# Kernel tuning notes

Hardware: AMD Instinct MI355X
Metric: run time of the kernel (lower is better)

Reference implementation:

```python
import jax, jax.numpy as jnp
import numpy as np

G = 8          # group (window) size -> N = G*G = 64
HEADS = 8
DIM = 256
HEAD_DIM = DIM // HEADS
SCALE = HEAD_DIM ** -0.5
POS_DIM = (DIM // 4) // 4  # 16
LN_EPS = 1e-5


def _make_bias_tables():
    # biases: coordinates (1-g..g-1) x (1-g..g-1) -> [(2g-1)^2, 2] float
    r = np.arange(1 - G, G)
    bh, bw = np.meshgrid(r, r, indexing='ij')
    biases = np.stack([bh.ravel(), bw.ravel()], axis=1).astype(np.float32)
    # relative position index [g^2, g^2]
    ch, cw = np.meshgrid(np.arange(G), np.arange(G), indexing='ij')
    coords = np.stack([ch.ravel(), cw.ravel()])              # [2, g^2]
    rel = coords[:, :, None] - coords[:, None, :]            # [2, g^2, g^2]
    rel = rel.transpose(1, 2, 0)
    rel[:, :, 0] += G - 1
    rel[:, :, 1] += G - 1
    rel[:, :, 0] *= 2 * G - 1
    rel_idx = rel.sum(-1).astype(np.int32)                   # [g^2, g^2]
    return biases, rel_idx


def setup_inputs() -> dict:
    key = jax.random.key(0)
    ks = jax.random.split(key, 8)
    B, N, C = 2048, G * G, DIM
    biases_np, rel_idx_np = _make_bias_tables()
    s = lambda fan: 1.0 / np.sqrt(fan)
    return {
        'x': jax.random.normal(ks[0], (B, N, C), jnp.float32),
        'qkv_w': jax.random.normal(ks[1], (C, 3 * C), jnp.float32) * s(C),
        'qkv_b': jnp.zeros((3 * C,), jnp.float32),
        'proj_w': jax.random.normal(ks[2], (C, C), jnp.float32) * s(C),
        'proj_b': jnp.zeros((C,), jnp.float32),
        'pos_proj_w': jax.random.normal(ks[3], (2, POS_DIM), jnp.float32) * s(2),
        'pos_proj_b': jnp.zeros((POS_DIM,), jnp.float32),
        'ln1_g': jnp.ones((POS_DIM,), jnp.float32), 'ln1_b': jnp.zeros((POS_DIM,), jnp.float32),
        'fc1_w': jax.random.normal(ks[4], (POS_DIM, POS_DIM), jnp.float32) * s(POS_DIM),
        'fc1_b': jnp.zeros((POS_DIM,), jnp.float32),
        'ln2_g': jnp.ones((POS_DIM,), jnp.float32), 'ln2_b': jnp.zeros((POS_DIM,), jnp.float32),
        'fc2_w': jax.random.normal(ks[5], (POS_DIM, POS_DIM), jnp.float32) * s(POS_DIM),
        'fc2_b': jnp.zeros((POS_DIM,), jnp.float32),
        'ln3_g': jnp.ones((POS_DIM,), jnp.float32), 'ln3_b': jnp.zeros((POS_DIM,), jnp.float32),
        'fc3_w': jax.random.normal(ks[6], (POS_DIM, HEADS), jnp.float32) * s(POS_DIM),
        'fc3_b': jnp.zeros((HEADS,), jnp.float32),
        'biases': jnp.asarray(biases_np),
        'rel_idx': jnp.asarray(rel_idx_np),
    }


def _ln(h, g, b):
    m = jnp.mean(h, -1, keepdims=True)
    v = jnp.mean((h - m) ** 2, -1, keepdims=True)
    return (h - m) * jax.lax.rsqrt(v + LN_EPS) * g + b


def reference(x, qkv_w, qkv_b, proj_w, proj_b,
              pos_proj_w, pos_proj_b,
              ln1_g, ln1_b, fc1_w, fc1_b,
              ln2_g, ln2_b, fc2_w, fc2_b,
              ln3_g, ln3_b, fc3_w, fc3_b,
              biases, rel_idx):
    B, N, C = x.shape
    # dynamic position bias MLP: [(2g-1)^2, 2] -> [(2g-1)^2, heads]
    h = biases @ pos_proj_w + pos_proj_b
    h = jax.nn.relu(_ln(h, ln1_g, ln1_b)) @ fc1_w + fc1_b
    h = jax.nn.relu(_ln(h, ln2_g, ln2_b)) @ fc2_w + fc2_b
    pos = jax.nn.relu(_ln(h, ln3_g, ln3_b)) @ fc3_w + fc3_b        # [225, H]
    rel_bias = pos[rel_idx]                                        # [N, N, H]
    rel_bias = jnp.transpose(rel_bias, (2, 0, 1))                  # [H, N, N]

    qkv = (x @ qkv_w + qkv_b).reshape(B, N, 3, HEADS, HEAD_DIM)
    qkv = jnp.transpose(qkv, (2, 0, 3, 1, 4))                      # [3, B, H, N, Dh]
    q, k, v = qkv[0] * SCALE, qkv[1], qkv[2]
    attn = jnp.einsum('bhnd,bhmd->bhnm', q, k) + rel_bias[None]    # [B, H, N, N]
    attn = jax.nn.softmax(attn, axis=-1)
    out = jnp.einsum('bhnm,bhmd->bhnd', attn, v)                   # [B, H, N, Dh]
    out = jnp.transpose(out, (0, 2, 1, 3)).reshape(B, N, C)
    return out @ proj_w + proj_b
```

## Files before the change

### kernel.cpp

```cpp
#include <hip/hip_runtime.h>

typedef _Float16 half_t;
typedef __attribute__((ext_vector_type(8))) _Float16 half8;
typedef __attribute__((ext_vector_type(4))) _Float16 half4;
typedef __attribute__((ext_vector_type(4))) float float4v;

#define LN_EPS 1e-5f
#define QK_SCALE 0.17677669529663687f

static __device__ __forceinline__ float4v mfma16(half8 a, half8 b, float4v c) {
    return __builtin_amdgcn_mfma_f32_16x16x32_f16(a, b, c, 0, 0, 0);
}

static __device__ __forceinline__ int swzA(int row, int colByte) {
    return row * 512 + ((((colByte >> 4) ^ ((row >> 1) & 7)) << 4) | (colByte & 15));
}
static __device__ __forceinline__ int swzB(int row, int colByte) {
    return row * 64 + ((((colByte >> 4) ^ ((row >> 1) & 3)) << 4) | (colByte & 15));
}
static __device__ __forceinline__ int swzC(int row, int colByte) {
    return row * 128 + ((((colByte >> 4) ^ (row & 7)) << 4) | (colByte & 15));
}

static __device__ void ln_relu16(float* h, const float* __restrict__ g, const float* __restrict__ b) {
    float m = 0.f;
    for (int j = 0; j < 16; ++j) m += h[j];
    m *= (1.0f / 16.0f);
    float v = 0.f;
    for (int j = 0; j < 16; ++j) { float d = h[j] - m; v += d * d; }
    v *= (1.0f / 16.0f);
    float rs = rsqrtf(v + LN_EPS);
    for (int j = 0; j < 16; ++j) {
        float t = (h[j] - m) * rs * g[j] + b[j];
        h[j] = t > 0.f ? t : 0.f;
    }
}

__global__ void prep_kernel(
    const float* __restrict__ qkv_w,
    const float* __restrict__ proj_w,
    const float* __restrict__ biases,
    const float* __restrict__ pos_w, const float* __restrict__ pos_b,
    const float* __restrict__ ln1_g, const float* __restrict__ ln1_b,
    const float* __restrict__ fc1_w, const float* __restrict__ fc1_b,
    const float* __restrict__ ln2_g, const float* __restrict__ ln2_b,
    const float* __restrict__ fc2_w, const float* __restrict__ fc2_b,
    const float* __restrict__ ln3_g, const float* __restrict__ ln3_b,
    const float* __restrict__ fc3_w, const float* __restrict__ fc3_b,
    const int* __restrict__ rel_idx,
    half_t* __restrict__ wqkvT,
    half_t* __restrict__ wprojT,
    float* __restrict__ rbp)
{
    __shared__ float tile[64][65];
    __shared__ float pos_s[225][8];
    const int t = blockIdx.x;
    const int tid = threadIdx.x;

    if (t < 64) {
        const float* src; half_t* dst; int ncols, rg, cg;
        if (t < 48) { src = qkv_w;  dst = wqkvT;  ncols = 768; rg = t / 12;      cg = t % 12; }
        else        { src = proj_w; dst = wprojT; ncols = 256; rg = (t-48) >> 2; cg = (t-48) & 3; }
        const int r0 = tid >> 6, c = tid & 63;
        for (int i = 0; i < 16; ++i) {
            int r = i * 4 + r0;
            tile[r][c] = src[(rg * 64 + r) * ncols + cg * 64 + c];
        }
        __syncthreads();
        for (int i = 0; i < 16; ++i) {
            int r = i * 4 + r0;
            dst[(cg * 64 + r) * 256 + rg * 64 + c] = (half_t)tile[c][r];
        }
    } else {
        if (tid < 225) {
            float h[16], h2[16];
            float b0 = biases[tid * 2], b1 = biases[tid * 2 + 1];
            for (int j = 0; j < 16; ++j) h[j] = b0 * pos_w[j] + b1 * pos_w[16 + j] + pos_b[j];
            ln_relu16(h, ln1_g, ln1_b);
            for (int j = 0; j < 16; ++j) {
                float s = fc1_b[j];
                for (int k = 0; k < 16; ++k) s += h[k] * fc1_w[k * 16 + j];
                h2[j] = s;
            }
            ln_relu16(h2, ln2_g, ln2_b);
            for (int j = 0; j < 16; ++j) {
                float s = fc2_b[j];
                for (int k = 0; k < 16; ++k) s += h2[k] * fc2_w[k * 16 + j];
                h[j] = s;
            }
            ln_relu16(h, ln3_g, ln3_b);
            for (int j = 0; j < 8; ++j) {
                float s = fc3_b[j];
                for (int k = 0; k < 16; ++k) s += h[k] * fc3_w[k * 8 + j];
                pos_s[tid][j] = s;
            }
        }
        __syncthreads();
        for (int e = tid; e < 8 * 64 * 64; e += 256) {
            int hh = e >> 12, rem = e & 4095;
            int row = rem >> 6, c = rem & 63;
            int tj = c >> 4, mm = c & 15;
            rbp[hh * 4096 + row * 64 + mm * 4 + tj] = pos_s[rel_idx[row * 64 + c]][hh];
        }
    }
}

__global__ __launch_bounds__(512, 2) void fused_kernel(
    const float* __restrict__ x,
    const half_t* __restrict__ wqkvT,
    const float* __restrict__ qkv_b,
    const half_t* __restrict__ wprojT,
    const float* __restrict__ proj_b,
    const float* __restrict__ rbp,
    float* __restrict__ out)
{
    __shared__ __align__(16) char smem[65536];
    char* xs  = smem;
    char* atn = smem;
    char* arenas = smem + 32768;

    const int b   = blockIdx.x;
    const int tid = threadIdx.x;
    const int w    = tid >> 6;
    const int lane = tid & 63;
    const int m = lane & 15;
    const int g = lane >> 4;
    char* wA  = arenas + w * 4096;
    char* vts = xs + w * 4096;

    const float* xg = x + (size_t)b * 16384;
    #pragma unroll
    for (int i = 0; i < 8; ++i) {
        int u = tid + i * 512;
        int row = u >> 6, c4 = u & 63;
        float4v xv = *(const float4v*)(xg + u * 4);
        half4 hv;
        hv[0] = (half_t)xv[0]; hv[1] = (half_t)xv[1];
        hv[2] = (half_t)xv[2]; hv[3] = (half_t)xv[3];
        *(half4*)(xs + swzA(row, c4 * 8)) = hv;
    }
    __syncthreads();

    float4v qb[2][2];
    #pragma unroll
    for (int pt = 0; pt < 2; ++pt)
        #pragma unroll
        for (int c2 = 0; c2 < 2; ++c2)
            qb[pt][c2] = *(const float4v*)(qkv_b + pt * 256 + w * 32 + c2 * 16 + g * 4);

    half8 aq[4], bk[4];
    {
        float4v qa[2][4], ka[2][4];
        #pragma unroll
        for (int c2 = 0; c2 < 2; ++c2)
            #pragma unroll
            for (int ti = 0; ti < 4; ++ti) {
                qa[c2][ti] = {0.f, 0.f, 0.f, 0.f};
                ka[c2][ti] = {0.f, 0.f, 0.f, 0.f};
            }
        const half_t* wqb = wqkvT + (size_t)(w * 32 + m) * 256 + g * 8;
        #pragma unroll
        for (int kk = 0; kk < 8; ++kk) {
            half8 af[4];
            #pragma unroll
            for (int ti = 0; ti < 4; ++ti)
                af[ti] = *(const half8*)(xs + swzA(ti * 16 + m, kk * 64 + g * 16));
            half8 wq0 = *(const half8*)(wqb + kk * 32);
            half8 wq1 = *(const half8*)(wqb + 16 * 256 + kk * 32);
            half8 wk0 = *(const half8*)(wqb + 256 * 256 + kk * 32);
            half8 wk1 = *(const half8*)(wqb + 272 * 256 + kk * 32);
            #pragma unroll
            for (int ti = 0; ti < 4; ++ti) {
                qa[0][ti] = mfma16(wq0, af[ti], qa[0][ti]);
                qa[1][ti] = mfma16(wq1, af[ti], qa[1][ti]);
                ka[0][ti] = mfma16(wk0, af[ti], ka[0][ti]);
                ka[1][ti] = mfma16(wk1, af[ti], ka[1][ti]);
            }
        }
        #pragma unroll
        for (int c2 = 0; c2 < 2; ++c2)
            #pragma unroll
            for (int ti = 0; ti < 4; ++ti) {
                half4 t;
                #pragma unroll
                for (int r = 0; r < 4; ++r) t[r] = (half_t)(qa[c2][ti][r] + qb[0][c2][r]);
                *(half4*)(wA + ti * 1024 + swzB(m, (c2 * 16 + g * 4) * 2)) = t;
            }
        #pragma unroll
        for (int ti = 0; ti < 4; ++ti)
            aq[ti] = *(const half8*)(wA + ti * 1024 + swzB(m, g * 16));
        __builtin_amdgcn_sched_barrier(0);
        #pragma unroll
        for (int c2 = 0; c2 < 2; ++c2)
            #pragma unroll
            for (int ti = 0; ti < 4; ++ti) {
                half4 t;
                #pragma unroll
                for (int r = 0; r < 4; ++r) t[r] = (half_t)(ka[c2][ti][r] + qb[1][c2][r]);
                *(half4*)(wA + ti * 1024 + swzB(m, (c2 * 16 + g * 4) * 2)) = t;
            }
        #pragma unroll
        for (int ti = 0; ti < 4; ++ti)
            bk[ti] = *(const half8*)(wA + ti * 1024 + swzB(m, g * 16));
        __builtin_amdgcn_sched_barrier(0);
    }

    half4 ph[4][4];
    const float* rbh = rbp + w * 4096;
    #pragma unroll
    for (int ti = 0; ti < 4; ++ti) {
        float4v z = {0.f, 0.f, 0.f, 0.f};
        float4v s0 = mfma16(aq[ti], bk[0], z);
        float4v s1 = mfma16(aq[ti], bk[1], z);
        float4v s2 = mfma16(aq[ti], bk[2], z);
        float4v s3 = mfma16(aq[ti], bk[3], z);
        #pragma unroll
        for (int r = 0; r < 4; ++r) {
            float4v rb = *(const float4v*)(rbh + (ti * 16 + g * 4 + r) * 64 + m * 4);
            float e0 = __expf(s0[r] * QK_SCALE + rb[0]);
            float e1 = __expf(s1[r] * QK_SCALE + rb[1]);
            float e2 = __expf(s2[r] * QK_SCALE + rb[2]);
            float e3 = __expf(s3[r] * QK_SCALE + rb[3]);
            float s = e0 + e1 + e2 + e3;
            s += __shfl_xor(s, 1); s += __shfl_xor(s, 2);
            s += __shfl_xor(s, 4); s += __shfl_xor(s, 8);
            float is = 1.0f / s;
            ph[ti][0][r] = (half_t)(e0 * is);
            ph[ti][1][r] = (half_t)(e1 * is);
            ph[ti][2][r] = (half_t)(e2 * is);
            ph[ti][3][r] = (half_t)(e3 * is);
        }
    }

    half4 vh[2][4];
    {
        float4v va[2][4];
        #pragma unroll
        for (int c2 = 0; c2 < 2; ++c2)
            #pragma unroll
            for (int ti = 0; ti < 4; ++ti) va[c2][ti] = {0.f, 0.f, 0.f, 0.f};
        const half_t* wvb = wqkvT + (size_t)(512 + w * 32 + m) * 256 + g * 8;
        #pragma unroll
        for (int kk = 0; kk < 8; ++kk) {
            half8 wv0 = *(const half8*)(wvb + kk * 32);
            half8 wv1 = *(const half8*)(wvb + 16 * 256 + kk * 32);
            #pragma unroll
            for (int ti = 0; ti < 4; ++ti) {
                half8 af = *(const half8*)(xs + swzA(ti * 16 + m, kk * 64 + g * 16));
                va[0][ti] = mfma16(af, wv0, va[0][ti]);
                va[1][ti] = mfma16(af, wv1, va[1][ti]);
            }
        }
        float vb0 = qkv_b[512 + w * 32 + m], vb1 = qkv_b[512 + w * 32 + 16 + m];
        #pragma unroll
        for (int c2 = 0; c2 < 2; ++c2)
            #pragma unroll
            for (int ti = 0; ti < 4; ++ti)
                #pragma unroll
                for (int r = 0; r < 4; ++r)
                    vh[c2][ti][r] = (half_t)(va[c2][ti][r] + (c2 ? vb1 : vb0));
    }
    __syncthreads();

    #pragma unroll
    for (int c2 = 0; c2 < 2; ++c2)
        #pragma unroll
        for (int ti = 0; ti < 4; ++ti)
            *(half4*)(vts + swzC(c2 * 16 + m, ti * 32 + g * 8)) = vh[c2][ti];

    float4v oacc[2][4];
    #pragma unroll
    for (int tjd = 0; tjd < 2; ++tjd)
        #pragma unroll
        for (int ti = 0; ti < 4; ++ti) oacc[tjd][ti] = {0.f, 0.f, 0.f, 0.f};
    #pragma unroll
    for (int nc = 0; nc < 2; ++nc) {
        #pragma unroll
        for (int ti = 0; ti < 4; ++ti)
            #pragma unroll
            for (int t2 = 0; t2 < 2; ++t2)
                #pragma unroll
                for (int r = 0; r < 4; ++r)
                    *(half_t*)(wA + swzB(ti * 16 + g * 4 + r, (t2 * 16 + m) * 2)) =
                        ph[ti][nc * 2 + t2][r];
        half8 pa[4];
        #pragma unroll
        for (int ti = 0; ti < 4; ++ti)
            pa[ti] = *(const half8*)(wA + swzB(ti * 16 + m, g * 16));
        #pragma unroll
        for (int tjd = 0; tjd < 2; ++tjd) {
            half8 bv = *(const half8*)(vts + swzC(tjd * 16 + m, nc * 64 + g * 16));
            #pragma unroll
            for (int ti = 0; ti < 4; ++ti)
                oacc[tjd][ti] = mfma16(pa[ti], bv, oacc[tjd][ti]);
        }
        __builtin_amdgcn_sched_barrier(0);
    }
    __syncthreads();

    #pragma unroll
    for (int tjd = 0; tjd < 2; ++tjd)
        #pragma unroll
        for (int ti = 0; ti < 4; ++ti)
            #pragma unroll
            for (int r = 0; r < 4; ++r)
                *(half_t*)(atn + swzA(ti * 16 + g * 4 + r, (w * 32 + tjd * 16 + m) * 2)) =
                    (half_t)oacc[tjd][ti][r];
    __syncthreads();

    float* og = out + (size_t)b * 16384;
    const int oc0 = w * 32;
    float4v pacc[2][4];
    #pragma unroll
    for (int c2 = 0; c2 < 2; ++c2)
        #pragma unroll
        for (int ti = 0; ti < 4; ++ti) pacc[c2][ti] = {0.f, 0.f, 0.f, 0.f};
    const half_t* wpb = wprojT + (size_t)(oc0 + m) * 256 + g * 8;
    #pragma unroll
    for (int kk = 0; kk < 8; ++kk) {
        half8 wf0 = *(const half8*)(wpb + kk * 32);
        half8 wf1 = *(const half8*)(wpb + 16 * 256 + kk * 32);
        #pragma unroll
        for (int ti = 0; ti < 4; ++ti) {
            half8 af = *(const half8*)(atn + swzA(ti * 16 + m, kk * 64 + g * 16));
            pacc[0][ti] = mfma16(af, wf0, pacc[0][ti]);
            pacc[1][ti] = mfma16(af, wf1, pacc[1][ti]);
        }
    }
    float pb0 = proj_b[oc0 + m], pb1 = proj_b[oc0 + 16 + m];
    #pragma unroll
    for (int c2 = 0; c2 < 2; ++c2)
        #pragma unroll
        for (int ti = 0; ti < 4; ++ti)
            #pragma unroll
            for (int r = 0; r < 4; ++r)
                og[(ti * 16 + g * 4 + r) * 256 + oc0 + c2 * 16 + m] =
                    pacc[c2][ti][r] + (c2 ? pb1 : pb0);
}

extern "C" void kernel_launch(void* const* d_in, const int* in_sizes, int n_in,
                              void* d_out, int out_size, void* d_ws, size_t ws_size,
                              hipStream_t stream) {
    const float* x          = (const float*)d_in[0];
    const float* qkv_w      = (const float*)d_in[1];
    const float* qkv_b      = (const float*)d_in[2];
    const float* proj_w     = (const float*)d_in[3];
    const float* proj_b     = (const float*)d_in[4];
    const float* pos_proj_w = (const float*)d_in[5];
    const float* pos_proj_b = (const float*)d_in[6];
    const float* ln1_g = (const float*)d_in[7];
    const float* ln1_b = (const float*)d_in[8];
    const float* fc1_w = (const float*)d_in[9];
    const float* fc1_b = (const float*)d_in[10];
    const float* ln2_g = (const float*)d_in[11];
    const float* ln2_b = (const float*)d_in[12];
    const float* fc2_w = (const float*)d_in[13];
    const float* fc2_b = (const float*)d_in[14];
    const float* ln3_g = (const float*)d_in[15];
    const float* ln3_b = (const float*)d_in[16];
    const float* fc3_w = (const float*)d_in[17];
    const float* fc3_b = (const float*)d_in[18];
    const float* biases = (const float*)d_in[19];
    const int*  rel_idx = (const int*)d_in[20];

    half_t* wqkvT  = (half_t*)d_ws;
    half_t* wprojT = (half_t*)((char*)d_ws + 393216);
    float*  rbp    = (float*)((char*)d_ws + 524288);

    const int B = in_sizes[0] / (64 * 256);

    prep_kernel<<<65, 256, 0, stream>>>(qkv_w, proj_w, biases, pos_proj_w, pos_proj_b,
                                        ln1_g, ln1_b, fc1_w, fc1_b,
                                        ln2_g, ln2_b, fc2_w, fc2_b,
                                        ln3_g, ln3_b, fc3_w, fc3_b,
                                        rel_idx, wqkvT, wprojT, rbp);
    fused_kernel<<<B, 512, 0, stream>>>(x, wqkvT, qkv_b, wprojT, proj_b, rbp,
                                        (float*)d_out);
}
```

Measured before the change: 264.2 us.

## Split fused attention into per-half-window QKV/attention kernel and separate projection kernel

```diff
diff --git a/kernel.cpp b/kernel.cpp
--- a/kernel.cpp
+++ b/kernel.cpp
@@ -105,7 +105,267 @@
     }
 }
 
-__global__ __launch_bounds__(512, 2) void fused_kernel(
+__global__ __launch_bounds__(256, 3) void qkv_attn_kernel(
+    const float* __restrict__ x,
+    const half_t* __restrict__ wqkvT,
+    const float* __restrict__ qkv_b,
+    const float* __restrict__ rbp,
+    half_t* __restrict__ attn_ws)
+{
+    __shared__ __align__(16) char smem[49152];
+    char* xs = smem;
+
+    const int bb  = blockIdx.x;
+    const int win = bb >> 1;
+    const int tid = threadIdx.x;
+    const int w    = tid >> 6;
+    const int h    = (bb & 1) * 4 + w;
+    const int lane = tid & 63;
+    const int m = lane & 15;
+    const int g = lane >> 4;
+    char* wA  = smem + 32768 + w * 4096;
+    char* vts = xs + w * 8192;
+
+    const float* xg = x + (size_t)win * 16384;
+    #pragma unroll
+    for (int i = 0; i < 16; ++i) {
+        int u = tid + i * 256;
+        int row = u >> 6, c4 = u & 63;
+        float4v xv = *(const float4v*)(xg + u * 4);
+        half4 hv;
+        hv[0] = (half_t)xv[0]; hv[1] = (half_t)xv[1];
+        hv[2] = (half_t)xv[2]; hv[3] = (half_t)xv[3];
+        *(half4*)(xs + swzA(row, c4 * 8)) = hv;
+    }
+    __syncthreads();
+
+    float4v qb[2][2];
+    #pragma unroll
+    for (int pt = 0; pt < 2; ++pt)
+        #pragma unroll
+        for (int c2 = 0; c2 < 2; ++c2)
+            qb[pt][c2] = *(const float4v*)(qkv_b + pt * 256 + h * 32 + c2 * 16 + g * 4);
+
+    half8 aq[4], bk[4];
+    {
+        float4v qa[2][4], ka[2][4];
+        #pragma unroll
+        for (int c2 = 0; c2 < 2; ++c2)
+            #pragma unroll
+            for (int ti = 0; ti < 4; ++ti) {
+                qa[c2][ti] = {0.f, 0.f, 0.f, 0.f};
+                ka[c2][ti] = {0.f, 0.f, 0.f, 0.f};
+            }
+        const half_t* wqb = wqkvT + (size_t)(h * 32 + m) * 256 + g * 8;
+        #pragma unroll
+        for (int kk = 0; kk < 8; ++kk) {
+            half8 af[4];
+            #pragma unroll
+            for (int ti = 0; ti < 4; ++ti)
+                af[ti] = *(const half8*)(xs + swzA(ti * 16 + m, kk * 64 + g * 16));
+            half8 wq0 = *(const half8*)(wqb + kk * 32);
+            half8 wq1 = *(const half8*)(wqb + 16 * 256 + kk * 32);
+            half8 wk0 = *(const half8*)(wqb + 256 * 256 + kk * 32);
+            half8 wk1 = *(const half8*)(wqb + 272 * 256 + kk * 32);
+            #pragma unroll
+            for (int ti = 0; ti < 4; ++ti) {
+                qa[0][ti] = mfma16(wq0, af[ti], qa[0][ti]);
+                qa[1][ti] = mfma16(wq1, af[ti], qa[1][ti]);
+                ka[0][ti] = mfma16(wk0, af[ti], ka[0][ti]);
+                ka[1][ti] = mfma16(wk1, af[ti], ka[1][ti]);
+            }
+        }
+        #pragma unroll
+        for (int c2 = 0; c2 < 2; ++c2)
+            #pragma unroll
+            for (int ti = 0; ti < 4; ++ti) {
+                half4 t;
+                #pragma unroll
+                for (int r = 0; r < 4; ++r) t[r] = (half_t)(qa[c2][ti][r] + qb[0][c2][r]);
+                *(half4*)(wA + ti * 1024 + swzB(m, (c2 * 16 + g * 4) * 2)) = t;
+            }
+        #pragma unroll
+        for (int ti = 0; ti < 4; ++ti)
+            aq[ti] = *(const half8*)(wA + ti * 1024 + swzB(m, g * 16));
+        __builtin_amdgcn_sched_barrier(0);
+        #pragma unroll
+        for (int c2 = 0; c2 < 2; ++c2)
+            #pragma unroll
+            for (int ti = 0; ti < 4; ++ti) {
+                half4 t;
+                #pragma unroll
+                for (int r = 0; r < 4; ++r) t[r] = (half_t)(ka[c2][ti][r] + qb[1][c2][r]);
+                *(half4*)(wA + ti * 1024 + swzB(m, (c2 * 16 + g * 4) * 2)) = t;
+            }
+        #pragma unroll
+        for (int ti = 0; ti < 4; ++ti)
+            bk[ti] = *(const half8*)(wA + ti * 1024 + swzB(m, g * 16));
+        __builtin_amdgcn_sched_barrier(0);
+    }
+
+    half4 ph[4][4];
+    const float* rbh = rbp + h * 4096;
+    #pragma unroll
+    for (int ti = 0; ti < 4; ++ti) {
+        float4v z = {0.f, 0.f, 0.f, 0.f};
+        float4v s0 = mfma16(aq[ti], bk[0], z);
+        float4v s1 = mfma16(aq[ti], bk[1], z);
+        float4v s2 = mfma16(aq[ti], bk[2], z);
+        float4v s3 = mfma16(aq[ti], bk[3], z);
+        #pragma unroll
+        for (int r = 0; r < 4; ++r) {
+            float4v rb = *(const float4v*)(rbh + (ti * 16 + g * 4 + r) * 64 + m * 4);
+            float e0 = __expf(s0[r] * QK_SCALE + rb[0]);
+            float e1 = __expf(s1[r] * QK_SCALE + rb[1]);
+            float e2 = __expf(s2[r] * QK_SCALE + rb[2]);
+            float e3 = __expf(s3[r] * QK_SCALE + rb[3]);
+            float s = e0 + e1 + e2 + e3;
+            s += __shfl_xor(s, 1); s += __shfl_xor(s, 2);
+            s += __shfl_xor(s, 4); s += __shfl_xor(s, 8);
+            float is = 1.0f / s;
+            ph[ti][0][r] = (half_t)(e0 * is);
+            ph[ti][1][r] = (half_t)(e1 * is);
+            ph[ti][2][r] = (half_t)(e2 * is);
+            ph[ti][3][r] = (half_t)(e3 * is);
+        }
+    }
+
+    half4 vh[2][4];
+    {
+        float4v va[2][4];
+        #pragma unroll
+        for (int c2 = 0; c2 < 2; ++c2)
+            #pragma unroll
+            for (int ti = 0; ti < 4; ++ti) va[c2][ti] = {0.f, 0.f, 0.f, 0.f};
+        const half_t* wvb = wqkvT + (size_t)(512 + h * 32 + m) * 256 + g * 8;
+        #pragma unroll
+        for (int kk = 0; kk < 8; ++kk) {
+            half8 wv0 = *(const half8*)(wvb + kk * 32);
+            half8 wv1 = *(const half8*)(wvb + 16 * 256 + kk * 32);
+            #pragma unroll
+            for (int ti = 0; ti < 4; ++ti) {
+                half8 af = *(const half8*)(xs + swzA(ti * 16 + m, kk * 64 + g * 16));
+                va[0][ti] = mfma16(af, wv0, va[0][ti]);
+                va[1][ti] = mfma16(af, wv1, va[1][ti]);
+            }
+        }
+        float vb0 = qkv_b[512 + h * 32 + m], vb1 = qkv_b[512 + h * 32 + 16 + m];
+        #pragma unroll
+        for (int c2 = 0; c2 < 2; ++c2)
+            #pragma unroll
+            for (int ti = 0; ti < 4; ++ti)
+                #pragma unroll
+                for (int r = 0; r < 4; ++r)
+                    vh[c2][ti][r] = (half_t)(va[c2][ti][r] + (c2 ? vb1 : vb0));
+    }
+    __syncthreads();
+
+    #pragma unroll
+    for (int c2 = 0; c2 < 2; ++c2)
+        #pragma unroll
+        for (int ti = 0; ti < 4; ++ti)
+            *(half4*)(vts + swzC(c2 * 16 + m, ti * 32 + g * 8)) = vh[c2][ti];
+
+    float4v oacc[2][4];
+    #pragma unroll
+    for (int tjd = 0; tjd < 2; ++tjd)
+        #pragma unroll
+        for (int ti = 0; ti < 4; ++ti) oacc[tjd][ti] = {0.f, 0.f, 0.f, 0.f};
+    #pragma unroll
+    for (int nc = 0; nc < 2; ++nc) {
+        #pragma unroll
+        for (int ti = 0; ti < 4; ++ti)
+            #pragma unroll
+            for (int t2 = 0; t2 < 2; ++t2)
+                #pragma unroll
+                for (int r = 0; r < 4; ++r)
+                    *(half_t*)(wA + swzB(ti * 16 + g * 4 + r, (t2 * 16 + m) * 2)) =
+                        ph[ti][nc * 2 + t2][r];
+        half8 pa[4];
+        #pragma unroll
+        for (int ti = 0; ti < 4; ++ti)
+            pa[ti] = *(const half8*)(wA + swzB(ti * 16 + m, g * 16));
+        #pragma unroll
+        for (int tjd = 0; tjd < 2; ++tjd) {
+            half8 bv = *(const half8*)(vts + swzC(tjd * 16 + m, nc * 64 + g * 16));
+            #pragma unroll
+            for (int ti = 0; ti < 4; ++ti)
+                oacc[tjd][ti] = mfma16(pa[ti], bv, oacc[tjd][ti]);
+        }
+        __builtin_amdgcn_sched_barrier(0);
+    }
+
+    half_t* ag = attn_ws + (size_t)win * 16384;
+    #pragma unroll
+    for (int tjd = 0; tjd < 2; ++tjd)
+        #pragma unroll
+        for (int ti = 0; ti < 4; ++ti)
+            #pragma unroll
+            for (int r = 0; r < 4; ++r)
+                ag[(ti * 16 + g * 4 + r) * 256 + h * 32 + tjd * 16 + m] =
+                    (half_t)oacc[tjd][ti][r];
+}
+
+__global__ __launch_bounds__(256, 4) void proj_kernel(
+    const half_t* __restrict__ attn_ws,
+    const half_t* __restrict__ wprojT,
+    const float* __restrict__ proj_b,
+    float* __restrict__ out)
+{
+    __shared__ __align__(16) char smem[32768];
+    char* xs = smem;
+
+    const int win = blockIdx.x;
+    const int tid = threadIdx.x;
+    const int w    = tid >> 6;
+    const int lane = tid & 63;
+    const int m = lane & 15;
+    const int g = lane >> 4;
+
+    const half_t* ag = attn_ws + (size_t)win * 16384;
+    #pragma unroll
+    for (int i = 0; i < 8; ++i) {
+        int u = tid + i * 256;
+        int row = u >> 5, c8 = u & 31;
+        half8 v = *(const half8*)(ag + u * 8);
+        *(half8*)(xs + swzA(row, c8 * 16)) = v;
+    }
+    __syncthreads();
+
+    float* og = out + (size_t)win * 16384;
+    #pragma unroll
+    for (int cp = 0; cp < 2; ++cp) {
+        const int oc0 = w * 64 + cp * 32;
+        float4v pacc[2][4];
+        #pragma unroll
+        for (int c2 = 0; c2 < 2; ++c2)
+            #pragma unroll
+            for (int ti = 0; ti < 4; ++ti) pacc[c2][ti] = {0.f, 0.f, 0.f, 0.f};
+        const half_t* wpb = wprojT + (size_t)(oc0 + m) * 256 + g * 8;
+        #pragma unroll
+        for (int kk = 0; kk < 8; ++kk) {
+            half8 wf0 = *(const half8*)(wpb + kk * 32);
+            half8 wf1 = *(const half8*)(wpb + 16 * 256 + kk * 32);
+            #pragma unroll
+            for (int ti = 0; ti < 4; ++ti) {
+                half8 af = *(const half8*)(xs + swzA(ti * 16 + m, kk * 64 + g * 16));
+                pacc[0][ti] = mfma16(af, wf0, pacc[0][ti]);
+                pacc[1][ti] = mfma16(af, wf1, pacc[1][ti]);
+            }
+        }
+        float pb0 = proj_b[oc0 + m], pb1 = proj_b[oc0 + 16 + m];
+        #pragma unroll
+        for (int c2 = 0; c2 < 2; ++c2)
+            #pragma unroll
+            for (int ti = 0; ti < 4; ++ti)
+                #pragma unroll
+                for (int r = 0; r < 4; ++r)
+                    og[(ti * 16 + g * 4 + r) * 256 + oc0 + c2 * 16 + m] =
+                        pacc[c2][ti][r] + (c2 ? pb1 : pb0);
+    }
+}
+
+__global__ __launch_bounds__(512, 2) void fused_fallback(
     const float* __restrict__ x,
     const half_t* __restrict__ wqkvT,
     const float* __restrict__ qkv_b,
@@ -366,14 +626,21 @@
     half_t* wqkvT  = (half_t*)d_ws;
     half_t* wprojT = (half_t*)((char*)d_ws + 393216);
     float*  rbp    = (float*)((char*)d_ws + 524288);
+    half_t* attn_ws = (half_t*)((char*)d_ws + 655360);
 
     const int B = in_sizes[0] / (64 * 256);
+    const size_t need = 655360 + (size_t)B * 64 * 256 * 2;
 
     prep_kernel<<<65, 256, 0, stream>>>(qkv_w, proj_w, biases, pos_proj_w, pos_proj_b,
                                         ln1_g, ln1_b, fc1_w, fc1_b,
                                         ln2_g, ln2_b, fc2_w, fc2_b,
                                         ln3_g, ln3_b, fc3_w, fc3_b,
                                         rel_idx, wqkvT, wprojT, rbp);
-    fused_kernel<<<B, 512, 0, stream>>>(x, wqkvT, qkv_b, wprojT, proj_b, rbp,
-                                        (float*)d_out);
-}
+    if (ws_size >= need) {
+        qkv_attn_kernel<<<B * 2, 256, 0, stream>>>(x, wqkvT, qkv_b, rbp, attn_ws);
+        proj_kernel<<<B, 256, 0, stream>>>(attn_ws, wprojT, proj_b, (float*)d_out);
+    } else {
+        fused_fallback<<<B, 512, 0, stream>>>(x, wqkvT, qkv_b, wprojT, proj_b, rbp,
+                                              (float*)d_out);
+    }
+}
```

Result: slower. 311.5 us (+17.9%).
